# Optimization experiments

Hardware: AMD Instinct MI355X
Metric: run time of the kernel (lower is better)

The kernel has to match this reference:

```python
import jax, jax.numpy as jnp
import numpy as np

NUM_HEADS = 16
EMBED_DIM = 1024
SEQ_LEN = 2048
BATCH = 2


def setup_inputs() -> dict:
    key = jax.random.key(0)
    ks = jax.random.split(key, 7)
    E = EMBED_DIM
    scale = 1.0 / np.sqrt(E)
    return {
        "query": jax.random.normal(ks[0], (SEQ_LEN, BATCH, E), jnp.float32),
        "key": jax.random.normal(ks[1], (SEQ_LEN, BATCH, E), jnp.float32),
        "value": jax.random.normal(ks[2], (SEQ_LEN, BATCH, E), jnp.float32),
        "in_proj_weight": jax.random.normal(ks[3], (3 * E, E), jnp.float32) * scale,
        "in_proj_bias": jnp.zeros((3 * E,), jnp.float32),
        "out_proj_weight": jax.random.normal(ks[4], (E, E), jnp.float32) * scale,
        "out_proj_bias": jnp.zeros((E,), jnp.float32),
    }


def reference(query, key, value, in_proj_weight, in_proj_bias, out_proj_weight, out_proj_bias):
    T, B, E = query.shape
    H = NUM_HEADS
    d = E // H
    scaling = float(d) ** -0.5
    # in-projections: rows [0:E) -> q, [E:2E) -> k, [2E:3E) -> v
    q = query @ in_proj_weight[:E].T + in_proj_bias[:E]
    k = key @ in_proj_weight[E:2 * E].T + in_proj_bias[E:2 * E]
    v = value @ in_proj_weight[2 * E:].T + in_proj_bias[2 * E:]
    q = q * scaling
    # (T, B, E) -> (B*H, T, d)
    q = q.reshape(T, B * H, d).transpose(1, 0, 2)
    k = k.reshape(T, B * H, d).transpose(1, 0, 2)
    v = v.reshape(T, B * H, d).transpose(1, 0, 2)
    S = k.shape[1]
    scores = jnp.einsum('ntd,nsd->nts', q, k)  # (B*H, T, S)
    attn = jax.nn.softmax(scores, axis=-1)
    out = jnp.einsum('nts,nsd->ntd', attn, v)  # (B*H, T, d)
    out = out.transpose(1, 0, 2).reshape(T, B, E)
    out = out @ out_proj_weight.T + out_proj_bias
    attn_avg = attn.reshape(B, H, T, S).sum(axis=1) / H
    return out, attn_avg
```

## Files before the change

### kernel.cpp

```cpp
#include <hip/hip_runtime.h>
#include <math.h>

#define T_LEN 2048
#define BATCH 2
#define EMB 1024
#define NHEAD 16
#define HDIM 64
#define BH (BATCH*NHEAD)
#define MROWS (T_LEN*BATCH)
#define QSCALE (0.125f * 1.4426950408889634f)
#define HEADBUF ((size_t)BH*T_LEN*HDIM)

typedef __attribute__((ext_vector_type(8))) short bf16x8;
typedef __attribute__((ext_vector_type(4))) float f32x4;

#define MFMA16(a,b,c) __builtin_amdgcn_mfma_f32_16x16x32_bf16(a,b,c,0,0,0)

__device__ __forceinline__ short f2bf(float f) {
    union { float f; unsigned u; } v; v.f = f;
    unsigned r = (v.u + 0x7FFFu + ((v.u >> 16) & 1u)) >> 16;
    return (short)(unsigned short)r;
}
__device__ __forceinline__ float bf2f(short s) {
    union { unsigned u; float f; } v; v.u = ((unsigned)(unsigned short)s) << 16;
    return v.f;
}
__device__ __forceinline__ unsigned cvtpk(float a, float b) {
    unsigned r;
    asm("v_cvt_pk_bf16_f32 %0, %1, %2" : "=v"(r) : "v"(a), "v"(b));
    return r;
}
__device__ __forceinline__ void gload16(const void* g, void* l) {
    __builtin_amdgcn_global_load_lds(
        (const __attribute__((address_space(1))) unsigned*)g,
        (__attribute__((address_space(3))) unsigned*)l, 16, 0, 0);
}

__global__ __launch_bounds__(256) void tobf16_kernel(
    const float* __restrict__ q, const float* __restrict__ k,
    const float* __restrict__ v, const float* __restrict__ w,
    const float* __restrict__ wo, short* __restrict__ out)
{
    size_t i8 = ((size_t)blockIdx.x * 256 + threadIdx.x) * 8;
    const float* src; size_t off;
    if (i8 < 12582912) {
        int sel = (int)(i8 >> 22);
        src = (sel == 0) ? q : (sel == 1) ? k : v;
        off = i8 & 4194303;
    } else if (i8 < 15728640) {
        src = w;  off = i8 - 12582912;
    } else {
        src = wo; off = i8 - 15728640;
    }
    float4 f0 = *(const float4*)(src + off);
    float4 f1 = *(const float4*)(src + off + 4);
    bf16x8 o;
    o[0]=f2bf(f0.x); o[1]=f2bf(f0.y); o[2]=f2bf(f0.z); o[3]=f2bf(f0.w);
    o[4]=f2bf(f1.x); o[5]=f2bf(f1.y); o[6]=f2bf(f1.z); o[7]=f2bf(f1.w);
    *(bf16x8*)(out + i8) = o;
}

__global__ __launch_bounds__(256) void inproj_gemm(
    const short* __restrict__ Xq, const short* __restrict__ Xk,
    const short* __restrict__ Xv, const short* __restrict__ Wb,
    const float* __restrict__ bias,
    short* __restrict__ qbuf, short* __restrict__ kbuf, short* __restrict__ vbufT)
{
    const int mBase = blockIdx.x * 128;
    const int nBase = blockIdx.y * 128;
    const int which = nBase >> 10;
    const short* __restrict__ X = (which == 0) ? Xq : (which == 1) ? Xk : Xv;

    __shared__ short Ast[2][128][32];
    __shared__ short Bst[2][128][32];

    const int tid  = threadIdx.x;
    const int lane = tid & 63;
    const int w    = tid >> 6;
    const int wr   = w >> 1, wc = w & 1;
    const int lr   = lane & 15, lg = lane >> 4;

    const int srow = lane >> 2;
    const int schk = (lane & 3) ^ ((lane >> 3) & 3);
    const int fchk = (lg ^ ((lr >> 1) & 3)) * 16;

    f32x4 acc[4][4] = {};

    #pragma unroll
    for (int j = 0; j < 2; ++j) {
        int r = j * 64 + w * 16 + srow;
        gload16(X  + (size_t)(mBase + r) * EMB + schk * 8,
                (char*)Ast[0] + j * 4096 + w * 1024);
        gload16(Wb + (size_t)(nBase + r) * EMB + schk * 8,
                (char*)Bst[0] + j * 4096 + w * 1024);
    }
    __syncthreads();

    int cur = 0;
    for (int kb = 0; kb < EMB; kb += 32) {
        if (kb + 32 < EMB) {
            #pragma unroll
            for (int j = 0; j < 2; ++j) {
                int r = j * 64 + w * 16 + srow;
                gload16(X  + (size_t)(mBase + r) * EMB + kb + 32 + schk * 8,
                        (char*)Ast[cur ^ 1] + j * 4096 + w * 1024);
                gload16(Wb + (size_t)(nBase + r) * EMB + kb + 32 + schk * 8,
                        (char*)Bst[cur ^ 1] + j * 4096 + w * 1024);
            }
        }
        bf16x8 af[4], bfr[4];
        #pragma unroll
        for (int rg = 0; rg < 4; ++rg)
            af[rg] = *(const bf16x8*)((char*)Ast[cur] + (wr * 64 + rg * 16 + lr) * 64 + fchk);
        #pragma unroll
        for (int cg = 0; cg < 4; ++cg)
            bfr[cg] = *(const bf16x8*)((char*)Bst[cur] + (wc * 64 + cg * 16 + lr) * 64 + fchk);
        #pragma unroll
        for (int rg = 0; rg < 4; ++rg)
            #pragma unroll
            for (int cg = 0; cg < 4; ++cg)
                acc[rg][cg] = MFMA16(af[rg], bfr[cg], acc[rg][cg]);
        __syncthreads();
        cur ^= 1;
    }

    #pragma unroll
    for (int rg = 0; rg < 4; ++rg) {
        #pragma unroll
        for (int cg = 0; cg < 4; ++cg) {
            int n  = nBase + wc * 64 + cg * 16 + lr;
            int e  = n & 1023;
            int h  = e >> 6, dd = e & 63;
            float bs = bias[n];
            #pragma unroll
            for (int ri = 0; ri < 4; ++ri) {
                int m = mBase + wr * 64 + rg * 16 + lg * 4 + ri;
                int t = m >> 1, b = m & 1;
                float val = acc[rg][cg][ri] + bs;
                short bfv;
                if (which == 0) { bfv = f2bf(val * QSCALE);
                    qbuf[((size_t)(b * NHEAD + h) * T_LEN + t) * HDIM + dd] = bfv; }
                else if (which == 1) { bfv = f2bf(val);
                    kbuf[((size_t)(b * NHEAD + h) * T_LEN + t) * HDIM + dd] = bfv; }
                else {
                    bfv = f2bf(val);
                    int s5 = t & 31;
                    int kk = ((s5 >> 2) & 3) * 8 + ((s5 >> 4) << 2) + (s5 & 3);
                    int tt = (t & ~31) | kk;
                    vbufT[((size_t)(b * NHEAD + h) * HDIM + dd) * T_LEN + tt] = bfv;
                }
            }
        }
    }
}

__global__ __launch_bounds__(256) void flash_kernel(
    const short* __restrict__ qb, const short* __restrict__ kbuf,
    const short* __restrict__ vbufT, short* __restrict__ h1,
    float* __restrict__ mlws)
{
    const int qt = blockIdx.x;
    const int hb = blockIdx.y;

    __shared__ short Kst[2][64][64];
    __shared__ short Vst[2][64][64];

    const int tid  = threadIdx.x;
    const int lane = tid & 63;
    const int w    = tid >> 6;
    const int lr   = lane & 15, lg = lane >> 4;

    bf16x8 qa0, qa1;
    {
        const short* qsrc = qb + ((size_t)hb * T_LEN + qt * 64 + w * 16 + lr) * HDIM;
        qa0 = *(const bf16x8*)(qsrc + lg * 8);
        qa1 = *(const bf16x8*)(qsrc + 32 + lg * 8);
    }

    const short* kbase = kbuf  + (size_t)hb * T_LEN * HDIM;
    const short* vbase = vbufT + (size_t)hb * HDIM * T_LEN;

    const int krow = lane >> 3;
    const int kc16 = (lane & 7) ^ krow;
    const int rb0 = ((0 + lg) ^ (lr & 7)) * 16;
    const int rb1 = ((4 + lg) ^ (lr & 7)) * 16;

    float l_r = 0.f;
    f32x4 o_acc[4] = {};

    for (int st = 0; st < T_LEN / 128; ++st) {
        __syncthreads();
        #pragma unroll
        for (int it = 0; it < 2; ++it) {
            int r = (w * 2 + it) * 8 + krow;
            #pragma unroll
            for (int sh = 0; sh < 2; ++sh) {
                gload16(kbase + (size_t)(st * 128 + sh * 64 + r) * HDIM + kc16 * 8,
                        (char*)Kst[sh] + (w * 2 + it) * 1024);
                gload16(vbase + (size_t)r * T_LEN + st * 128 + sh * 64 + kc16 * 8,
                        (char*)Vst[sh] + (w * 2 + it) * 1024);
            }
        }
        __syncthreads();

        #pragma unroll
        for (int sh = 0; sh < 2; ++sh) {
            f32x4 sc[4] = {};
            #pragma unroll
            for (int sg = 0; sg < 4; ++sg) {
                const char* krowp = (const char*)Kst[sh] + (sg * 16 + lr) * 128;
                bf16x8 kf0 = *(const bf16x8*)(krowp + rb0);
                bf16x8 kf1 = *(const bf16x8*)(krowp + rb1);
                sc[sg] = MFMA16(kf0, qa0, sc[sg]);
                sc[sg] = MFMA16(kf1, qa1, sc[sg]);
            }

            float p[4][4];
            #pragma unroll
            for (int sg = 0; sg < 4; ++sg)
                #pragma unroll
                for (int ri = 0; ri < 4; ++ri) {
                    p[sg][ri] = exp2f(sc[sg][ri]);
                    l_r += p[sg][ri];
                }

            #pragma unroll
            for (int ks = 0; ks < 2; ++ks) {
                union { unsigned u[4]; bf16x8 v; } pau;
                pau.u[0] = cvtpk(p[ks * 2][0],     p[ks * 2][1]);
                pau.u[1] = cvtpk(p[ks * 2][2],     p[ks * 2][3]);
                pau.u[2] = cvtpk(p[ks * 2 + 1][0], p[ks * 2 + 1][1]);
                pau.u[3] = cvtpk(p[ks * 2 + 1][2], p[ks * 2 + 1][3]);
                #pragma unroll
                for (int dsub = 0; dsub < 4; ++dsub) {
                    const char* vrowp = (const char*)Vst[sh] + (dsub * 16 + lr) * 128;
                    bf16x8 vf = *(const bf16x8*)(vrowp + (ks ? rb1 : rb0));
                    o_acc[dsub] = MFMA16(pau.v, vf, o_acc[dsub]);
                }
            }
        }
    }

    float lsum = l_r;
    lsum += __shfl_xor(lsum, 16);
    lsum += __shfl_xor(lsum, 32);
    float inv = 1.0f / lsum;
    float invq[4];
    #pragma unroll
    for (int ri = 0; ri < 4; ++ri) invq[ri] = __shfl(inv, lg * 20 + ri);
    #pragma unroll
    for (int ri = 0; ri < 4; ++ri) {
        int row = qt * 64 + w * 16 + lg * 4 + ri;
        #pragma unroll
        for (int dsub = 0; dsub < 4; ++dsub) {
            float x = o_acc[dsub][ri] * invq[ri];
            h1[((size_t)hb * T_LEN + row) * HDIM + dsub * 16 + lr] = f2bf(x);
        }
    }
    if (lg == 0) {
        int row = qt * 64 + w * 16 + lr;
        mlws[(size_t)hb * T_LEN + row] = __log2f(lsum);
    }
}

__global__ __launch_bounds__(256) void avg_kernel(
    const short* __restrict__ qbuf, const short* __restrict__ kbuf,
    const float* __restrict__ mlws, float* __restrict__ attn_avg)
{
    const int st  = blockIdx.x;
    const int qt2 = blockIdx.y;
    const int b   = blockIdx.z;

    __shared__ short K2[2][2][64][64];

    const int tid  = threadIdx.x;
    const int lane = tid & 63;
    const int w    = tid >> 6;
    const int lr   = lane & 15, lg = lane >> 4;
    const int srow = tid >> 3;
    const int scol = (tid & 7) * 8;

    f32x4 acc[2][4] = {};

    #pragma unroll
    for (int hh = 0; hh < 2; ++hh) {
        int hb0 = b * NHEAD + hh;
        #pragma unroll
        for (int j = 0; j < 2; ++j)
            gload16(kbuf + ((size_t)hb0 * T_LEN + st * 64 + j * 32 + srow) * HDIM + scol,
                    (char*)K2[0][hh] + j * 4096 + w * 1024);
    }
    __syncthreads();

    int cur = 0;
    for (int rnd = 0; rnd < 8; ++rnd) {
        if (rnd + 1 < 8) {
            #pragma unroll
            for (int hh = 0; hh < 2; ++hh) {
                int hbn = b * NHEAD + (rnd + 1) * 2 + hh;
                #pragma unroll
                for (int j = 0; j < 2; ++j)
                    gload16(kbuf + ((size_t)hbn * T_LEN + st * 64 + j * 32 + srow) * HDIM + scol,
                            (char*)K2[cur ^ 1][hh] + j * 4096 + w * 1024);
            }
        }
        #pragma unroll
        for (int hh = 0; hh < 2; ++hh) {
            int hb = b * NHEAD + rnd * 2 + hh;
            bf16x8 qa[2][2];
            #pragma unroll
            for (int qf = 0; qf < 2; ++qf) {
                const short* qsrc = qbuf +
                    ((size_t)hb * T_LEN + qt2 * 128 + qf * 64 + w * 16 + lr) * HDIM;
                qa[qf][0] = *(const bf16x8*)(qsrc + lg * 8);
                qa[qf][1] = *(const bf16x8*)(qsrc + 32 + lg * 8);
            }

            f32x4 sc[2][4] = {};
            __builtin_amdgcn_s_setprio(1);
            #pragma unroll
            for (int sg = 0; sg < 4; ++sg) {
                bf16x8 kf0 = *(const bf16x8*)&K2[cur][hh][sg * 16 + lr][lg * 8];
                bf16x8 kf1 = *(const bf16x8*)&K2[cur][hh][sg * 16 + lr][32 + lg * 8];
                #pragma unroll
                for (int qf = 0; qf < 2; ++qf) {
                    sc[qf][sg] = MFMA16(qa[qf][0], kf0, sc[qf][sg]);
                    sc[qf][sg] = MFMA16(qa[qf][1], kf1, sc[qf][sg]);
                }
            }
            __builtin_amdgcn_s_setprio(0);

            #pragma unroll
            for (int qf = 0; qf < 2; ++qf)
                #pragma unroll
                for (int ri = 0; ri < 4; ++ri) {
                    int row = qt2 * 128 + qf * 64 + w * 16 + lg * 4 + ri;
                    float ml = mlws[(size_t)hb * T_LEN + row];
                    #pragma unroll
                    for (int sg = 0; sg < 4; ++sg)
                        acc[qf][sg][ri] += exp2f(sc[qf][sg][ri] - ml);
                }
        }
        __syncthreads();
        cur ^= 1;
    }

    const float invH = 1.0f / (float)NHEAD;
    #pragma unroll
    for (int qf = 0; qf < 2; ++qf)
        #pragma unroll
        for (int ri = 0; ri < 4; ++ri) {
            int row = qt2 * 128 + qf * 64 + w * 16 + lg * 4 + ri;
            #pragma unroll
            for (int sg = 0; sg < 4; ++sg)
                attn_avg[((size_t)b * T_LEN + row) * T_LEN + st * 64 + sg * 16 + lr] =
                    acc[qf][sg][ri] * invH;
        }
}

__global__ __launch_bounds__(256) void outproj_gemm(
    const short* __restrict__ h1, const short* __restrict__ Wob,
    const float* __restrict__ bo, float* __restrict__ out)
{
    const int mBase = blockIdx.x * 128;
    const int nBase = blockIdx.y * 128;

    __shared__ short Ast[2][128][32];
    __shared__ short Bst[2][128][32];

    const int tid  = threadIdx.x;
    const int lane = tid & 63;
    const int w    = tid >> 6;
    const int wr   = w >> 1, wc = w & 1;
    const int lr   = lane & 15, lg = lane >> 4;

    const int srow = lane >> 2;
    const int schk = (lane & 3) ^ ((lane >> 3) & 3);
    const int fchk = (lg ^ ((lr >> 1) & 3)) * 16;

    f32x4 acc[4][4] = {};

    #define ASRC(r, kb)                                                       \
        (h1 + ((size_t)(((mBase + (r)) & 1) * NHEAD + ((kb) >> 6)) * T_LEN +  \
               ((mBase + (r)) >> 1)) * HDIM + ((kb) & 63) + schk * 8)

    #pragma unroll
    for (int j = 0; j < 2; ++j) {
        int r = j * 64 + w * 16 + srow;
        gload16(ASRC(r, 0), (char*)Ast[0] + j * 4096 + w * 1024);
        gload16(Wob + (size_t)(nBase + r) * EMB + schk * 8,
                (char*)Bst[0] + j * 4096 + w * 1024);
    }
    __syncthreads();

    int cur = 0;
    for (int kb = 0; kb < EMB; kb += 32) {
        if (kb + 32 < EMB) {
            #pragma unroll
            for (int j = 0; j < 2; ++j) {
                int r = j * 64 + w * 16 + srow;
                gload16(ASRC(r, kb + 32), (char*)Ast[cur ^ 1] + j * 4096 + w * 1024);
                gload16(Wob + (size_t)(nBase + r) * EMB + kb + 32 + schk * 8,
                        (char*)Bst[cur ^ 1] + j * 4096 + w * 1024);
            }
        }
        bf16x8 af[4], bfr[4];
        #pragma unroll
        for (int rg = 0; rg < 4; ++rg)
            af[rg] = *(const bf16x8*)((char*)Ast[cur] + (wr * 64 + rg * 16 + lr) * 64 + fchk);
        #pragma unroll
        for (int cg = 0; cg < 4; ++cg)
            bfr[cg] = *(const bf16x8*)((char*)Bst[cur] + (wc * 64 + cg * 16 + lr) * 64 + fchk);
        #pragma unroll
        for (int rg = 0; rg < 4; ++rg)
            #pragma unroll
            for (int cg = 0; cg < 4; ++cg)
                acc[rg][cg] = MFMA16(af[rg], bfr[cg], acc[rg][cg]);
        __syncthreads();
        cur ^= 1;
    }
    #undef ASRC

    #pragma unroll
    for (int rg = 0; rg < 4; ++rg) {
        #pragma unroll
        for (int cg = 0; cg < 4; ++cg) {
            int n = nBase + wc * 64 + cg * 16 + lr;
            float bs = bo[n];
            #pragma unroll
            for (int ri = 0; ri < 4; ++ri) {
                int m = mBase + wr * 64 + rg * 16 + lg * 4 + ri;
                out[(size_t)m * EMB + n] = acc[rg][cg][ri] + bs;
            }
        }
    }
}

extern "C" void kernel_launch(void* const* d_in, const int* in_sizes, int n_in,
                              void* d_out, int out_size, void* d_ws, size_t ws_size,
                              hipStream_t stream)
{
    const float* query = (const float*)d_in[0];
    const float* key   = (const float*)d_in[1];
    const float* value = (const float*)d_in[2];
    const float* ipw   = (const float*)d_in[3];
    const float* ipb   = (const float*)d_in[4];
    const float* opw   = (const float*)d_in[5];
    const float* opb   = (const float*)d_in[6];

    short* qb  = (short*)d_ws;
    short* kb  = qb + HEADBUF;
    short* vbT = kb + HEADBUF;
    short* h1  = vbT + HEADBUF;
    short* h2  = h1 + HEADBUF;
    short* xvb = h2 + HEADBUF;
    short* wbf = xvb + HEADBUF;
    short* wob = wbf + (size_t)3 * EMB * EMB;
    float* mlws = (float*)(wob + (size_t)EMB * EMB);

    float* out      = (float*)d_out;
    float* attn_avg = out + (size_t)MROWS * EMB;

    tobf16_kernel<<<8192, 256, 0, stream>>>(query, key, value, ipw, opw, h1);
    inproj_gemm  <<<dim3(MROWS / 128, 3 * EMB / 128), 256, 0, stream>>>(
        h1, h2, xvb, wbf, ipb, qb, kb, vbT);
    flash_kernel <<<dim3(T_LEN / 64, BH),             256, 0, stream>>>(
        qb, kb, vbT, h1, mlws);
    avg_kernel   <<<dim3(T_LEN / 64, T_LEN / 128, BATCH), 256, 0, stream>>>(
        qb, kb, mlws, attn_avg);
    outproj_gemm <<<dim3(MROWS / 128, EMB / 128),     256, 0, stream>>>(
        h1, wob, opb, out);
}
```

Baseline: 206.1 us.

## Swizzle K tile in LDS and shrink avg kernel query tile to 64

The head-averaged attention kernel now stages K into shared memory with an XOR swizzle on 16-byte chunks, and fragment reads use the matching swizzled offsets. The goal is to avoid LDS bank conflicts when reading K fragments. Each block now handles 64 query rows instead of 128, which doubles the grid and halves accumulator registers per thread to improve occupancy. In exchange, every K tile is loaded twice as often from global memory, since reuse across query rows drops.

```diff
diff --git a/kernel.cpp b/kernel.cpp
--- a/kernel.cpp
+++ b/kernel.cpp
@@ -267,9 +267,9 @@
     const short* __restrict__ qbuf, const short* __restrict__ kbuf,
     const float* __restrict__ mlws, float* __restrict__ attn_avg)
 {
-    const int st  = blockIdx.x;
-    const int qt2 = blockIdx.y;
-    const int b   = blockIdx.z;
+    const int st = blockIdx.x;
+    const int qt = blockIdx.y;
+    const int b  = blockIdx.z;
 
     __shared__ short K2[2][2][64][64];
 
@@ -277,18 +277,22 @@
     const int lane = tid & 63;
     const int w    = tid >> 6;
     const int lr   = lane & 15, lg = lane >> 4;
-    const int srow = tid >> 3;
-    const int scol = (tid & 7) * 8;
-
-    f32x4 acc[2][4] = {};
+
+    const int krow = lane >> 3;
+    const int kc16 = (lane & 7) ^ krow;
+    const int rb0 = ((0 + lg) ^ (lr & 7)) * 16;
+    const int rb1 = ((4 + lg) ^ (lr & 7)) * 16;
+
+    f32x4 acc[4] = {};
 
     #pragma unroll
     for (int hh = 0; hh < 2; ++hh) {
-        int hb0 = b * NHEAD + hh;
-        #pragma unroll
-        for (int j = 0; j < 2; ++j)
-            gload16(kbuf + ((size_t)hb0 * T_LEN + st * 64 + j * 32 + srow) * HDIM + scol,
-                    (char*)K2[0][hh] + j * 4096 + w * 1024);
+        #pragma unroll
+        for (int it = 0; it < 2; ++it) {
+            int r = (w * 2 + it) * 8 + krow;
+            gload16(kbuf + ((size_t)(b * NHEAD + hh) * T_LEN + st * 64 + r) * HDIM + kc16 * 8,
+                    (char*)K2[0][hh] + (w * 2 + it) * 1024);
+        }
     }
     __syncthreads();
 
@@ -299,47 +303,40 @@
             for (int hh = 0; hh < 2; ++hh) {
                 int hbn = b * NHEAD + (rnd + 1) * 2 + hh;
                 #pragma unroll
-                for (int j = 0; j < 2; ++j)
-                    gload16(kbuf + ((size_t)hbn * T_LEN + st * 64 + j * 32 + srow) * HDIM + scol,
-                            (char*)K2[cur ^ 1][hh] + j * 4096 + w * 1024);
+                for (int it = 0; it < 2; ++it) {
+                    int r = (w * 2 + it) * 8 + krow;
+                    gload16(kbuf + ((size_t)hbn * T_LEN + st * 64 + r) * HDIM + kc16 * 8,
+                            (char*)K2[cur ^ 1][hh] + (w * 2 + it) * 1024);
+                }
             }
         }
         #pragma unroll
         for (int hh = 0; hh < 2; ++hh) {
             int hb = b * NHEAD + rnd * 2 + hh;
-            bf16x8 qa[2][2];
-            #pragma unroll
-            for (int qf = 0; qf < 2; ++qf) {
-                const short* qsrc = qbuf +
-                    ((size_t)hb * T_LEN + qt2 * 128 + qf * 64 + w * 16 + lr) * HDIM;
-                qa[qf][0] = *(const bf16x8*)(qsrc + lg * 8);
-                qa[qf][1] = *(const bf16x8*)(qsrc + 32 + lg * 8);
-            }
-
-            f32x4 sc[2][4] = {};
+            const short* qsrc = qbuf + ((size_t)hb * T_LEN + qt * 64 + w * 16 + lr) * HDIM;
+            bf16x8 qa0 = *(const bf16x8*)(qsrc + lg * 8);
+            bf16x8 qa1 = *(const bf16x8*)(qsrc + 32 + lg * 8);
+
+            f32x4 sc[4] = {};
             __builtin_amdgcn_s_setprio(1);
             #pragma unroll
             for (int sg = 0; sg < 4; ++sg) {
-                bf16x8 kf0 = *(const bf16x8*)&K2[cur][hh][sg * 16 + lr][lg * 8];
-                bf16x8 kf1 = *(const bf16x8*)&K2[cur][hh][sg * 16 + lr][32 + lg * 8];
+                const char* krowp = (const char*)K2[cur][hh] + (sg * 16 + lr) * 128;
+                bf16x8 kf0 = *(const bf16x8*)(krowp + rb0);
+                bf16x8 kf1 = *(const bf16x8*)(krowp + rb1);
+                sc[sg] = MFMA16(qa0, kf0, sc[sg]);
+                sc[sg] = MFMA16(qa1, kf1, sc[sg]);
+            }
+            __builtin_amdgcn_s_setprio(0);
+
+            #pragma unroll
+            for (int ri = 0; ri < 4; ++ri) {
+                int row = qt * 64 + w * 16 + lg * 4 + ri;
+                float ml = mlws[(size_t)hb * T_LEN + row];
                 #pragma unroll
-                for (int qf = 0; qf < 2; ++qf) {
-                    sc[qf][sg] = MFMA16(qa[qf][0], kf0, sc[qf][sg]);
-                    sc[qf][sg] = MFMA16(qa[qf][1], kf1, sc[qf][sg]);
-                }
-            }
-            __builtin_amdgcn_s_setprio(0);
-
-            #pragma unroll
-            for (int qf = 0; qf < 2; ++qf)
-                #pragma unroll
-                for (int ri = 0; ri < 4; ++ri) {
-                    int row = qt2 * 128 + qf * 64 + w * 16 + lg * 4 + ri;
-                    float ml = mlws[(size_t)hb * T_LEN + row];
-                    #pragma unroll
-                    for (int sg = 0; sg < 4; ++sg)
-                        acc[qf][sg][ri] += exp2f(sc[qf][sg][ri] - ml);
-                }
+                for (int sg = 0; sg < 4; ++sg)
+                    acc[sg][ri] += exp2f(sc[sg][ri] - ml);
+            }
         }
         __syncthreads();
         cur ^= 1;
@@ -347,15 +344,13 @@
 
     const float invH = 1.0f / (float)NHEAD;
     #pragma unroll
-    for (int qf = 0; qf < 2; ++qf)
-        #pragma unroll
-        for (int ri = 0; ri < 4; ++ri) {
-            int row = qt2 * 128 + qf * 64 + w * 16 + lg * 4 + ri;
-            #pragma unroll
-            for (int sg = 0; sg < 4; ++sg)
-                attn_avg[((size_t)b * T_LEN + row) * T_LEN + st * 64 + sg * 16 + lr] =
-                    acc[qf][sg][ri] * invH;
-        }
+    for (int ri = 0; ri < 4; ++ri) {
+        int row = qt * 64 + w * 16 + lg * 4 + ri;
+        #pragma unroll
+        for (int sg = 0; sg < 4; ++sg)
+            attn_avg[((size_t)b * T_LEN + row) * T_LEN + st * 64 + sg * 16 + lr] =
+                acc[sg][ri] * invH;
+    }
 }
 
 __global__ __launch_bounds__(256) void outproj_gemm(
@@ -466,7 +461,7 @@
         h1, h2, xvb, wbf, ipb, qb, kb, vbT);
     flash_kernel <<<dim3(T_LEN / 64, BH),             256, 0, stream>>>(
         qb, kb, vbT, h1, mlws);
-    avg_kernel   <<<dim3(T_LEN / 64, T_LEN / 128, BATCH), 256, 0, stream>>>(
+    avg_kernel   <<<dim3(T_LEN / 64, T_LEN / 64, BATCH), 256, 0, stream>>>(
         qb, kb, mlws, attn_avg);
     outproj_gemm <<<dim3(MROWS / 128, EMB / 128),     256, 0, stream>>>(
         h1, wob, opb, out);
```

Result: faster. 196.6 us (median of 3 runs) (-4.6%).
